# Optimization experiments

Hardware: AMD Instinct MI355X
Metric: run time of the kernel (lower is better)

The kernel has to match this reference:

```python
import jax, jax.numpy as jnp
import numpy as np

B, N, C, P = 16, 4096, 4, 64
D = 128        # conv output channels (fixed in module)
WIN = 7        # window_size
ALPHA = 0.5
EPS = 1e-5     # BatchNorm eps


def setup_inputs() -> dict:
    key = jax.random.key(0)
    k1, k2, k3, k4 = jax.random.split(key, 4)
    x = jax.random.normal(k1, (B, N, C, P), jnp.float32)
    x_template = jax.random.normal(k2, (B, N, C, P), jnp.float32)
    # Conv1d(n_channel, 128, kernel_size=n_pts): weight [128, C, P], bias [128]
    W = jax.random.normal(k3, (D, C, P), jnp.float32) * 0.05
    b = jax.random.normal(k4, (D,), jnp.float32) * 0.01
    gamma = jnp.ones((D,), jnp.float32)   # BN weight init = 1
    beta = jnp.zeros((D,), jnp.float32)   # BN bias init = 0
    return {"x": x, "x_template": x_template, "W": W, "b": b, "gamma": gamma, "beta": beta}


def _embed(x_flat, W, b, gamma, beta):
    # Conv1d with kernel_size == full length -> contraction over (C, P), output length 1.
    h = jnp.einsum('ncp,dcp->nd', x_flat, W) + b           # [B*N, D]
    # BatchNorm1d in training mode: per-channel stats over the (B*N, L=1) batch.
    mean = h.mean(axis=0)
    var = h.var(axis=0)                                     # biased variance (torch BN)
    h = (h - mean) / jnp.sqrt(var + EPS) * gamma + beta
    return jnp.where(h >= 0, h, 0.1 * h)                    # LeakyReLU(0.1)


def reference(x, x_template, W, b, gamma, beta):
    nb, nc, ch, npt = x.shape
    hw = WIN // 2
    off = jnp.arange(-hw, hw + 1)
    raw = jnp.arange(nc)[:, None] + off[None, :]
    valid = (raw >= 0) & (raw < nc)                         # dedups clamped edge cols (matches dense mask)
    cols = jnp.clip(raw, 0, nc - 1)

    emb_x = _embed(x.reshape(nb * nc, ch, npt), W, b, gamma, beta).reshape(nb, nc, D)
    emb_t = _embed(x_template.reshape(nb * nc, ch, npt), W, b, gamma, beta).reshape(nb, nc, D)

    # Banded similarity: only the window entries the module actually uses.
    emb_t_win = emb_t[:, cols]
    sim = jnp.einsum('bnd,bnwd->bnw', emb_x, emb_t_win)

    # feat_fused = raw sim gathered at clamped window inds (duplicates at edges kept)
    feat_fused = sim

    # Masked softmax over the window (invalid = clamped duplicates excluded, as in dense mask)
    mx = jnp.where(valid, sim, -jnp.inf).max(axis=-1, keepdims=True)
    e = jnp.where(valid, jnp.exp(sim - mx), 0.0)
    attn = e / e.sum(axis=-1, keepdims=True)

    xt_flat = x_template.reshape(nb, nc, ch * npt)
    out = jnp.einsum('bnw,bnwe->bne', attn, xt_flat[:, cols])  # [B, N, C*P]
    out = out.reshape(nb, nc, ch, npt)
    out = ALPHA * x + (1.0 - ALPHA) * out
    return out, feat_fused
```

## Files before the change

### kernel.cpp

```cpp
#include <hip/hip_runtime.h>
#include <math.h>

#define BB 16
#define NN 4096
#define DD 128
#define KK 256
#define NROWS (BB*NN)
#define WIN 7
#define HWIN 3
#define ALPHA 0.5f
#define EPS 1e-5f

typedef __attribute__((ext_vector_type(8))) short bf16x8;
typedef __attribute__((ext_vector_type(4))) float f32x4;

__device__ __forceinline__ unsigned short f2b(float f) {
    unsigned u = __float_as_uint(f);
    u += 0x7FFFu + ((u >> 16) & 1u);
    return (unsigned short)(u >> 16);
}
__device__ __forceinline__ float b2f(unsigned short s) {
    return __uint_as_float(((unsigned)s) << 16);
}
__device__ __forceinline__ float b2f_lo(unsigned v) { return __uint_as_float(v << 16); }
__device__ __forceinline__ float b2f_hi(unsigned v) { return __uint_as_float(v & 0xFFFF0000u); }
__device__ __forceinline__ float lrelu(float v) { return v >= 0.f ? v : 0.1f * v; }

__global__ __launch_bounds__(256) void k_embed_mfma(
    const float* __restrict__ x,
    const float* __restrict__ xt,
    const float* __restrict__ W,
    const float* __restrict__ bvec,
    unsigned short* __restrict__ h_out,
    float* __restrict__ sums)
{
    __shared__ unsigned short Wsh[128 * 128];
    __shared__ unsigned short Xsh[64 * 128];

    const int blk  = blockIdx.x;
    const int src  = blk >> 10;
    const int tile = blk & 1023;
    const int row0 = tile * 64;
    const float* __restrict__ X = src ? xt : x;
    unsigned short* __restrict__ H = h_out + (size_t)src * NROWS * DD;

    const int t    = threadIdx.x;
    const int lane = t & 63;
    const int w    = t >> 6;
    const int wm   = w >> 1;
    const int wn   = w & 1;

    f32x4 acc[2][4];
    #pragma unroll
    for (int m = 0; m < 2; ++m)
        #pragma unroll
        for (int n = 0; n < 4; ++n)
            #pragma unroll
            for (int j = 0; j < 4; ++j) acc[m][n][j] = 0.f;

    #pragma unroll
    for (int ph = 0; ph < 2; ++ph) {
        #pragma unroll
        for (int p = 0; p < 8; ++p) {
            const int j  = t + p * 256;
            const int r  = j >> 4, k8 = j & 15;
            const float* gp = &W[(size_t)r * KK + ph * 128 + k8 * 8];
            const float4 a = *(const float4*)(gp);
            const float4 bq = *(const float4*)(gp + 4);
            uint4 v;
            v.x = (unsigned)f2b(a.x)  | ((unsigned)f2b(a.y)  << 16);
            v.y = (unsigned)f2b(a.z)  | ((unsigned)f2b(a.w)  << 16);
            v.z = (unsigned)f2b(bq.x) | ((unsigned)f2b(bq.y) << 16);
            v.w = (unsigned)f2b(bq.z) | ((unsigned)f2b(bq.w) << 16);
            const int off = r * 256 + ((k8 * 16) ^ ((r & 7) << 4));
            *(uint4*)((char*)Wsh + off) = v;
        }
        #pragma unroll
        for (int p = 0; p < 4; ++p) {
            const int j  = t + p * 256;
            const int r  = j >> 4, k8 = j & 15;
            const float* gp = &X[(size_t)(row0 + r) * KK + ph * 128 + k8 * 8];
            const float4 a = *(const float4*)(gp);
            const float4 bq = *(const float4*)(gp + 4);
            uint4 v;
            v.x = (unsigned)f2b(a.x)  | ((unsigned)f2b(a.y)  << 16);
            v.y = (unsigned)f2b(a.z)  | ((unsigned)f2b(a.w)  << 16);
            v.z = (unsigned)f2b(bq.x) | ((unsigned)f2b(bq.y) << 16);
            v.w = (unsigned)f2b(bq.z) | ((unsigned)f2b(bq.w) << 16);
            const int off = r * 256 + ((k8 * 16) ^ ((r & 7) << 4));
            *(uint4*)((char*)Xsh + off) = v;
        }
        __syncthreads();

        #pragma unroll
        for (int kk = 0; kk < 4; ++kk) {
            const int kb = kk * 64 + ((lane >> 4) << 4);
            bf16x8 af[2], bfr[4];
            #pragma unroll
            for (int m = 0; m < 2; ++m) {
                const int r = 32 * wm + 16 * m + (lane & 15);
                af[m] = *(const bf16x8*)((const char*)Xsh + r * 256 + (kb ^ ((r & 7) << 4)));
            }
            #pragma unroll
            for (int n = 0; n < 4; ++n) {
                const int d = 64 * wn + 16 * n + (lane & 15);
                bfr[n] = *(const bf16x8*)((const char*)Wsh + d * 256 + (kb ^ ((d & 7) << 4)));
            }
            #pragma unroll
            for (int m = 0; m < 2; ++m)
                #pragma unroll
                for (int n = 0; n < 4; ++n)
                    acc[m][n] = __builtin_amdgcn_mfma_f32_16x16x32_bf16(af[m], bfr[n], acc[m][n], 0, 0, 0);
        }
        __syncthreads();
    }

    const int csub = (lane & 15);
    float bv[4];
    #pragma unroll
    for (int n = 0; n < 4; ++n) bv[n] = bvec[64 * wn + 16 * n + csub];

    float s[4] = {0.f, 0.f, 0.f, 0.f}, q[4] = {0.f, 0.f, 0.f, 0.f};
    #pragma unroll
    for (int m = 0; m < 2; ++m) {
        #pragma unroll
        for (int j = 0; j < 4; ++j) {
            const int row = row0 + 32 * wm + 16 * m + ((lane >> 4) << 2) + j;
            #pragma unroll
            for (int n = 0; n < 4; ++n) {
                const float v = acc[m][n][j] + bv[n];
                H[(size_t)row * DD + 64 * wn + 16 * n + csub] = f2b(v);
                s[n] += v;
                q[n] += v * v;
            }
        }
    }
    #pragma unroll
    for (int n = 0; n < 4; ++n) {
        s[n] += __shfl_xor(s[n], 16); s[n] += __shfl_xor(s[n], 32);
        q[n] += __shfl_xor(q[n], 16); q[n] += __shfl_xor(q[n], 32);
    }
    float* red = (float*)Xsh;
    if (lane < 16) {
        #pragma unroll
        for (int n = 0; n < 4; ++n) {
            red[w * 64 + n * 16 + lane]       = s[n];
            red[256 + w * 64 + n * 16 + lane] = q[n];
        }
    }
    __syncthreads();
    if (t < 128) {
        const int c = t, i = c & 63, vn = c >> 6;
        const float S = red[vn * 64 + i] + red[(2 + vn) * 64 + i];
        const float Q = red[256 + vn * 64 + i] + red[256 + (2 + vn) * 64 + i];
        atomicAdd(&sums[src * 256 + c], S);
        atomicAdd(&sums[src * 256 + 128 + c], Q);
    }
}

__global__ void k_stats(const float* __restrict__ sums,
                        const float* __restrict__ gamma,
                        const float* __restrict__ beta,
                        float* __restrict__ ss)
{
    const int t = threadIdx.x;
    if (t < 256) {
        const int src = t >> 7;
        const int d   = t & 127;
        const float invn = 1.0f / (float)NROWS;
        const float mean = sums[src * 256 + d] * invn;
        const float var  = sums[src * 256 + 128 + d] * invn - mean * mean;
        const float sc   = gamma[d] / sqrtf(var + EPS);
        const float sh   = beta[d] - mean * sc;
        ss[src * 256 + d]       = sc;
        ss[src * 256 + 128 + d] = sh;
    }
}

__global__ __launch_bounds__(256) void k_attn(
    const float* __restrict__ x,
    const float* __restrict__ xt,
    const unsigned short* __restrict__ h,
    const float* __restrict__ ss,
    float* __restrict__ out,
    float* __restrict__ feat)
{
    const int blk  = blockIdx.x;
    const int bb   = blk >> 7;
    const int tile = blk & 127;
    const int n0   = tile * 32;
    const int t    = threadIdx.x;

    __shared__ float ex[32][132];
    __shared__ float et[38][132];
    __shared__ float attn[32][8];

    const unsigned short* __restrict__ Hx = h;
    const unsigned short* __restrict__ Ht = h + (size_t)NROWS * DD;
    const size_t rowbase = (size_t)bb * NN;

    #pragma unroll
    for (int p = 0; p < 2; ++p) {
        const int j = t + p * 256;
        const int r = j >> 4, c8 = j & 15;
        const uint4 u = *(const uint4*)(&Hx[(rowbase + n0 + r) * DD + c8 * 8]);
        const float4 sca = *(const float4*)(&ss[c8 * 8]);
        const float4 scb = *(const float4*)(&ss[c8 * 8 + 4]);
        const float4 sha = *(const float4*)(&ss[128 + c8 * 8]);
        const float4 shb = *(const float4*)(&ss[128 + c8 * 8 + 4]);
        float* dst = &ex[r][c8 * 8];
        dst[0] = lrelu(b2f_lo(u.x) * sca.x + sha.x);
        dst[1] = lrelu(b2f_hi(u.x) * sca.y + sha.y);
        dst[2] = lrelu(b2f_lo(u.y) * sca.z + sha.z);
        dst[3] = lrelu(b2f_hi(u.y) * sca.w + sha.w);
        dst[4] = lrelu(b2f_lo(u.z) * scb.x + shb.x);
        dst[5] = lrelu(b2f_hi(u.z) * scb.y + shb.y);
        dst[6] = lrelu(b2f_lo(u.w) * scb.z + shb.z);
        dst[7] = lrelu(b2f_hi(u.w) * scb.w + shb.w);
    }
    #pragma unroll
    for (int p = 0; p < 3; ++p) {
        const int j = t + p * 256;
        if (j < 608) {
            const int r = j >> 4, c8 = j & 15;
            int g = n0 - HWIN + r;
            g = min(max(g, 0), NN - 1);
            const uint4 u = *(const uint4*)(&Ht[(rowbase + g) * DD + c8 * 8]);
            const float4 sca = *(const float4*)(&ss[256 + c8 * 8]);
            const float4 scb = *(const float4*)(&ss[256 + c8 * 8 + 4]);
            const float4 sha = *(const float4*)(&ss[384 + c8 * 8]);
            const float4 shb = *(const float4*)(&ss[384 + c8 * 8 + 4]);
            float* dst = &et[r][c8 * 8];
            dst[0] = lrelu(b2f_lo(u.x) * sca.x + sha.x);
            dst[1] = lrelu(b2f_hi(u.x) * sca.y + sha.y);
            dst[2] = lrelu(b2f_lo(u.y) * sca.z + sha.z);
            dst[3] = lrelu(b2f_hi(u.y) * sca.w + sha.w);
            dst[4] = lrelu(b2f_lo(u.z) * scb.x + shb.x);
            dst[5] = lrelu(b2f_hi(u.z) * scb.y + shb.y);
            dst[6] = lrelu(b2f_lo(u.w) * scb.z + shb.z);
            dst[7] = lrelu(b2f_hi(u.w) * scb.w + shb.w);
        }
    }
    __syncthreads();

    if (t < 224) {
        const int n_i = t / 7;
        const int wv  = t % 7;
        const float* a = &ex[n_i][0];
        const float* b = &et[n_i + wv][0];
        float acc = 0.f;
        #pragma unroll
        for (int d4 = 0; d4 < 128; d4 += 4) {
            const float4 av = *(const float4*)(a + d4);
            const float4 bv = *(const float4*)(b + d4);
            acc += av.x * bv.x + av.y * bv.y + av.z * bv.z + av.w * bv.w;
        }
        feat[(rowbase + n0 + n_i) * WIN + wv] = acc;
        attn[n_i][wv] = acc;
    }
    __syncthreads();

    if (t < 32) {
        const int n = n0 + t;
        float mx = -1e30f;
        #pragma unroll
        for (int wv = 0; wv < WIN; ++wv) {
            const int c = n + wv - HWIN;
            if (c >= 0 && c < NN) mx = fmaxf(mx, attn[t][wv]);
        }
        float e[WIN];
        float esum = 0.f;
        #pragma unroll
        for (int wv = 0; wv < WIN; ++wv) {
            const int c = n + wv - HWIN;
            const bool valid = (c >= 0 && c < NN);
            e[wv] = valid ? expf(attn[t][wv] - mx) : 0.f;
            esum += e[wv];
        }
        const float inv = 1.0f / esum;
        #pragma unroll
        for (int wv = 0; wv < WIN; ++wv) attn[t][wv] = e[wv] * inv;
    }
    __syncthreads();

    #pragma unroll
    for (int p = 0; p < 8; ++p) {
        const int idx = t + p * 256;
        const int n_i = idx >> 6, e4 = idx & 63;
        const int n = n0 + n_i;
        const float4 xv = *(const float4*)(&x[(rowbase + n) * KK + e4 * 4]);
        float4 acc = make_float4(0.f, 0.f, 0.f, 0.f);
        #pragma unroll
        for (int wv = 0; wv < WIN; ++wv) {
            int g = n + wv - HWIN;
            g = min(max(g, 0), NN - 1);
            const float aw = attn[n_i][wv];
            const float4 tv = *(const float4*)(&xt[(rowbase + g) * KK + e4 * 4]);
            acc.x += aw * tv.x;
            acc.y += aw * tv.y;
            acc.z += aw * tv.z;
            acc.w += aw * tv.w;
        }
        float4 o;
        o.x = ALPHA * xv.x + (1.f - ALPHA) * acc.x;
        o.y = ALPHA * xv.y + (1.f - ALPHA) * acc.y;
        o.z = ALPHA * xv.z + (1.f - ALPHA) * acc.z;
        o.w = ALPHA * xv.w + (1.f - ALPHA) * acc.w;
        *(float4*)(&out[(rowbase + n) * KK + e4 * 4]) = o;
    }
}

extern "C" void kernel_launch(void* const* d_in, const int* in_sizes, int n_in,
                              void* d_out, int out_size, void* d_ws, size_t ws_size,
                              hipStream_t stream) {
    const float* x     = (const float*)d_in[0];
    const float* xt    = (const float*)d_in[1];
    const float* W     = (const float*)d_in[2];
    const float* bvec  = (const float*)d_in[3];
    const float* gamma = (const float*)d_in[4];
    const float* beta  = (const float*)d_in[5];

    float* out  = (float*)d_out;
    float* feat = out + (size_t)BB * NN * KK;

    char*  ws   = (char*)d_ws;
    unsigned short* h = (unsigned short*)ws;
    float* sums = (float*)(ws + (size_t)33554432);
    float* ss   = (float*)(ws + (size_t)33556480);

    hipMemsetAsync(sums, 0, 512 * sizeof(float), stream);
    k_embed_mfma<<<2048, 256, 0, stream>>>(x, xt, W, bvec, h, sums);
    k_stats<<<1, 256, 0, stream>>>(sums, gamma, beta, ss);
    k_attn<<<2048, 256, 0, stream>>>(x, xt, h, ss, out, feat);
}
```

Before: 237.5 us.

## Persistent double-buffered embed GEMM with register-resident weights; stage template in LDS

A small prep kernel converts W to swizzled bf16 once. The embed kernel now runs 256 blocks of 512 threads. Each block keeps its W fragments in registers and loops over eight 64-row X tiles, staging the next tile into a second LDS buffer while it computes the current one. This removes the per-block repeated W conversion and cuts the atomic count. In the attention kernel, the template rows for the window are staged once into LDS as bf16, overlapped with the softmax warp. This replaces seven redundant global fp32 reads per output element, but it lowers the precision of the weighted sum to bf16.

```diff
diff --git a/kernel.cpp b/kernel.cpp
--- a/kernel.cpp
+++ b/kernel.cpp
@@ -19,142 +19,161 @@
     u += 0x7FFFu + ((u >> 16) & 1u);
     return (unsigned short)(u >> 16);
 }
-__device__ __forceinline__ float b2f(unsigned short s) {
-    return __uint_as_float(((unsigned)s) << 16);
-}
 __device__ __forceinline__ float b2f_lo(unsigned v) { return __uint_as_float(v << 16); }
 __device__ __forceinline__ float b2f_hi(unsigned v) { return __uint_as_float(v & 0xFFFF0000u); }
 __device__ __forceinline__ float lrelu(float v) { return v >= 0.f ? v : 0.1f * v; }
 
-__global__ __launch_bounds__(256) void k_embed_mfma(
+__device__ __forceinline__ uint4 pack8(float4 a, float4 b) {
+    uint4 v;
+    v.x = (unsigned)f2b(a.x)  | ((unsigned)f2b(a.y)  << 16);
+    v.y = (unsigned)f2b(a.z)  | ((unsigned)f2b(a.w)  << 16);
+    v.z = (unsigned)f2b(b.x)  | ((unsigned)f2b(b.y)  << 16);
+    v.w = (unsigned)f2b(b.z)  | ((unsigned)f2b(b.w)  << 16);
+    return v;
+}
+
+__global__ __launch_bounds__(256) void k_prep(
+    const float* __restrict__ W, unsigned char* __restrict__ Wswz)
+{
+    const int id = blockIdx.x * 256 + threadIdx.x;
+    const int d  = id >> 5, c8 = id & 31;
+    const float4 a = *(const float4*)(&W[(size_t)d * KK + c8 * 8]);
+    const float4 b = *(const float4*)(&W[(size_t)d * KK + c8 * 8 + 4]);
+    const int off = d * 512 + ((c8 * 16) ^ ((d & 7) << 4));
+    *(uint4*)(Wswz + off) = pack8(a, b);
+}
+
+__device__ __forceinline__ void stage_x(const float* __restrict__ X, int grow0,
+                                        unsigned short* dst, int t)
+{
+    #pragma unroll
+    for (int p = 0; p < 4; ++p) {
+        const int j  = t + p * 512;
+        const int r  = j >> 5, c8 = j & 31;
+        const float* gp = X + (size_t)(grow0 + r) * KK + c8 * 8;
+        const float4 a = *(const float4*)(gp);
+        const float4 b = *(const float4*)(gp + 4);
+        const int off = r * 512 + ((c8 * 16) ^ ((r & 7) << 4));
+        *(uint4*)((char*)dst + off) = pack8(a, b);
+    }
+}
+
+__global__ __launch_bounds__(512) void k_embed(
     const float* __restrict__ x,
     const float* __restrict__ xt,
-    const float* __restrict__ W,
+    const uint4* __restrict__ Wswz,
     const float* __restrict__ bvec,
     unsigned short* __restrict__ h_out,
     float* __restrict__ sums)
 {
-    __shared__ unsigned short Wsh[128 * 128];
-    __shared__ unsigned short Xsh[64 * 128];
+    __shared__ unsigned short Wsh[128 * 256];
+    __shared__ unsigned short Xs[2][64 * 256];
 
     const int blk  = blockIdx.x;
-    const int src  = blk >> 10;
-    const int tile = blk & 1023;
-    const int row0 = tile * 64;
+    const int src  = blk >> 7;
+    const int tile = blk & 127;
+    const int row0 = tile * 512;
     const float* __restrict__ X = src ? xt : x;
     unsigned short* __restrict__ H = h_out + (size_t)src * NROWS * DD;
 
     const int t    = threadIdx.x;
     const int lane = t & 63;
     const int w    = t >> 6;
-    const int wm   = w >> 1;
-    const int wn   = w & 1;
-
-    f32x4 acc[2][4];
-    #pragma unroll
-    for (int m = 0; m < 2; ++m)
-        #pragma unroll
-        for (int n = 0; n < 4; ++n)
+    const int wm   = w & 1;
+    const int wn   = w >> 1;
+    const int l15  = lane & 15;
+    const int lg   = lane >> 4;
+
+    {
+        uint4* d4 = (uint4*)Wsh;
+        #pragma unroll
+        for (int p = 0; p < 8; ++p) d4[t + p * 512] = Wswz[t + p * 512];
+    }
+    stage_x(X, row0, &Xs[0][0], t);
+    __syncthreads();
+
+    bf16x8 breg[2][8];
+    #pragma unroll
+    for (int n = 0; n < 2; ++n) {
+        const int d = 32 * wn + 16 * n + l15;
+        #pragma unroll
+        for (int k = 0; k < 8; ++k) {
+            const int addr = d * 512 + (((k * 64) + lg * 16) ^ ((d & 7) << 4));
+            breg[n][k] = *(const bf16x8*)((const char*)Wsh + addr);
+        }
+    }
+
+    const float bv0 = bvec[32 * wn + l15];
+    const float bv1 = bvec[32 * wn + 16 + l15];
+    float s0 = 0.f, s1 = 0.f, q0 = 0.f, q1 = 0.f;
+
+    for (int st = 0; st < 8; ++st) {
+        const int cur = st & 1;
+        f32x4 acc[2][2];
+        #pragma unroll
+        for (int m = 0; m < 2; ++m)
             #pragma unroll
-            for (int j = 0; j < 4; ++j) acc[m][n][j] = 0.f;
-
-    #pragma unroll
-    for (int ph = 0; ph < 2; ++ph) {
-        #pragma unroll
-        for (int p = 0; p < 8; ++p) {
-            const int j  = t + p * 256;
-            const int r  = j >> 4, k8 = j & 15;
-            const float* gp = &W[(size_t)r * KK + ph * 128 + k8 * 8];
-            const float4 a = *(const float4*)(gp);
-            const float4 bq = *(const float4*)(gp + 4);
-            uint4 v;
-            v.x = (unsigned)f2b(a.x)  | ((unsigned)f2b(a.y)  << 16);
-            v.y = (unsigned)f2b(a.z)  | ((unsigned)f2b(a.w)  << 16);
-            v.z = (unsigned)f2b(bq.x) | ((unsigned)f2b(bq.y) << 16);
-            v.w = (unsigned)f2b(bq.z) | ((unsigned)f2b(bq.w) << 16);
-            const int off = r * 256 + ((k8 * 16) ^ ((r & 7) << 4));
-            *(uint4*)((char*)Wsh + off) = v;
-        }
-        #pragma unroll
-        for (int p = 0; p < 4; ++p) {
-            const int j  = t + p * 256;
-            const int r  = j >> 4, k8 = j & 15;
-            const float* gp = &X[(size_t)(row0 + r) * KK + ph * 128 + k8 * 8];
-            const float4 a = *(const float4*)(gp);
-            const float4 bq = *(const float4*)(gp + 4);
-            uint4 v;
-            v.x = (unsigned)f2b(a.x)  | ((unsigned)f2b(a.y)  << 16);
-            v.y = (unsigned)f2b(a.z)  | ((unsigned)f2b(a.w)  << 16);
-            v.z = (unsigned)f2b(bq.x) | ((unsigned)f2b(bq.y) << 16);
-            v.w = (unsigned)f2b(bq.z) | ((unsigned)f2b(bq.w) << 16);
-            const int off = r * 256 + ((k8 * 16) ^ ((r & 7) << 4));
-            *(uint4*)((char*)Xsh + off) = v;
-        }
-        __syncthreads();
-
-        #pragma unroll
-        for (int kk = 0; kk < 4; ++kk) {
-            const int kb = kk * 64 + ((lane >> 4) << 4);
-            bf16x8 af[2], bfr[4];
+            for (int n = 0; n < 2; ++n)
+                #pragma unroll
+                for (int j = 0; j < 4; ++j) acc[m][n][j] = 0.f;
+
+        const char* xb = (const char*)&Xs[cur][0];
+        #pragma unroll
+        for (int k = 0; k < 8; ++k) {
+            bf16x8 af[2];
             #pragma unroll
             for (int m = 0; m < 2; ++m) {
-                const int r = 32 * wm + 16 * m + (lane & 15);
-                af[m] = *(const bf16x8*)((const char*)Xsh + r * 256 + (kb ^ ((r & 7) << 4)));
+                const int r = 32 * wm + 16 * m + l15;
+                const int addr = r * 512 + (((k * 64) + lg * 16) ^ ((r & 7) << 4));
+                af[m] = *(const bf16x8*)(xb + addr);
             }
+            acc[0][0] = __builtin_amdgcn_mfma_f32_16x16x32_bf16(af[0], breg[0][k], acc[0][0], 0, 0, 0);
+            acc[0][1] = __builtin_amdgcn_mfma_f32_16x16x32_bf16(af[0], breg[1][k], acc[0][1], 0, 0, 0);
+            acc[1][0] = __builtin_amdgcn_mfma_f32_16x16x32_bf16(af[1], breg[0][k], acc[1][0], 0, 0, 0);
+            acc[1][1] = __builtin_amdgcn_mfma_f32_16x16x32_bf16(af[1], breg[1][k], acc[1][1], 0, 0, 0);
+        }
+
+        if (st < 7) stage_x(X, row0 + (st + 1) * 64, &Xs[cur ^ 1][0], t);
+
+        #pragma unroll
+        for (int m = 0; m < 2; ++m) {
             #pragma unroll
-            for (int n = 0; n < 4; ++n) {
-                const int d = 64 * wn + 16 * n + (lane & 15);
-                bfr[n] = *(const bf16x8*)((const char*)Wsh + d * 256 + (kb ^ ((d & 7) << 4)));
+            for (int j = 0; j < 4; ++j) {
+                const int row = row0 + st * 64 + 32 * wm + 16 * m + lg * 4 + j;
+                const float v0 = acc[m][0][j] + bv0;
+                const float v1 = acc[m][1][j] + bv1;
+                H[(size_t)row * DD + 32 * wn + l15]      = f2b(v0);
+                H[(size_t)row * DD + 32 * wn + 16 + l15] = f2b(v1);
+                s0 += v0; q0 += v0 * v0;
+                s1 += v1; q1 += v1 * v1;
             }
-            #pragma unroll
-            for (int m = 0; m < 2; ++m)
-                #pragma unroll
-                for (int n = 0; n < 4; ++n)
-                    acc[m][n] = __builtin_amdgcn_mfma_f32_16x16x32_bf16(af[m], bfr[n], acc[m][n], 0, 0, 0);
         }
         __syncthreads();
     }
 
-    const int csub = (lane & 15);
-    float bv[4];
-    #pragma unroll
-    for (int n = 0; n < 4; ++n) bv[n] = bvec[64 * wn + 16 * n + csub];
-
-    float s[4] = {0.f, 0.f, 0.f, 0.f}, q[4] = {0.f, 0.f, 0.f, 0.f};
-    #pragma unroll
-    for (int m = 0; m < 2; ++m) {
-        #pragma unroll
-        for (int j = 0; j < 4; ++j) {
-            const int row = row0 + 32 * wm + 16 * m + ((lane >> 4) << 2) + j;
-            #pragma unroll
-            for (int n = 0; n < 4; ++n) {
-                const float v = acc[m][n][j] + bv[n];
-                H[(size_t)row * DD + 64 * wn + 16 * n + csub] = f2b(v);
-                s[n] += v;
-                q[n] += v * v;
-            }
-        }
-    }
-    #pragma unroll
-    for (int n = 0; n < 4; ++n) {
-        s[n] += __shfl_xor(s[n], 16); s[n] += __shfl_xor(s[n], 32);
-        q[n] += __shfl_xor(q[n], 16); q[n] += __shfl_xor(q[n], 32);
-    }
-    float* red = (float*)Xsh;
+    s0 += __shfl_xor(s0, 16); s0 += __shfl_xor(s0, 32);
+    s1 += __shfl_xor(s1, 16); s1 += __shfl_xor(s1, 32);
+    q0 += __shfl_xor(q0, 16); q0 += __shfl_xor(q0, 32);
+    q1 += __shfl_xor(q1, 16); q1 += __shfl_xor(q1, 32);
+    float* red = (float*)Wsh;
     if (lane < 16) {
-        #pragma unroll
-        for (int n = 0; n < 4; ++n) {
-            red[w * 64 + n * 16 + lane]       = s[n];
-            red[256 + w * 64 + n * 16 + lane] = q[n];
-        }
+        red[(w * 2 + 0) * 16 + l15]       = s0;
+        red[(w * 2 + 1) * 16 + l15]       = s1;
+        red[256 + (w * 2 + 0) * 16 + l15] = q0;
+        red[256 + (w * 2 + 1) * 16 + l15] = q1;
     }
     __syncthreads();
     if (t < 128) {
-        const int c = t, i = c & 63, vn = c >> 6;
-        const float S = red[vn * 64 + i] + red[(2 + vn) * 64 + i];
-        const float Q = red[256 + vn * 64 + i] + red[256 + (2 + vn) * 64 + i];
-        atomicAdd(&sums[src * 256 + c], S);
-        atomicAdd(&sums[src * 256 + 128 + c], Q);
+        const int wn_ = t >> 5, n_ = (t >> 4) & 1, li = t & 15;
+        float S = 0.f, Q = 0.f;
+        #pragma unroll
+        for (int wm_ = 0; wm_ < 2; ++wm_) {
+            const int w_ = wn_ * 2 + wm_;
+            S += red[(w_ * 2 + n_) * 16 + li];
+            Q += red[256 + (w_ * 2 + n_) * 16 + li];
+        }
+        atomicAdd(&sums[src * 256 + t], S);
+        atomicAdd(&sums[src * 256 + 128 + t], Q);
     }
 }
 
@@ -193,7 +212,7 @@
 
     __shared__ float ex[32][132];
     __shared__ float et[38][132];
-    __shared__ float attn[32][8];
+    __shared__ float attnw[32][8];
 
     const unsigned short* __restrict__ Hx = h;
     const unsigned short* __restrict__ Ht = h + (size_t)NROWS * DD;
@@ -256,17 +275,33 @@
             acc += av.x * bv.x + av.y * bv.y + av.z * bv.z + av.w * bv.w;
         }
         feat[(rowbase + n0 + n_i) * WIN + wv] = acc;
-        attn[n_i][wv] = acc;
-    }
-    __syncthreads();
-
-    if (t < 32) {
-        const int n = n0 + t;
+        attnw[n_i][wv] = acc;
+    }
+    __syncthreads();
+
+    unsigned short* xts = (unsigned short*)&et[0][0];
+    if (t < 224) {
+        #pragma unroll
+        for (int p = 0; p < 6; ++p) {
+            const int j = t + p * 224;
+            if (j < 1216) {
+                const int r = j >> 5, c8 = j & 31;
+                int g = n0 - HWIN + r;
+                g = min(max(g, 0), NN - 1);
+                const float* gp = &xt[(rowbase + g) * KK + c8 * 8];
+                const float4 a = *(const float4*)(gp);
+                const float4 b = *(const float4*)(gp + 4);
+                *(uint4*)((char*)xts + r * 512 + c8 * 16) = pack8(a, b);
+            }
+        }
+    } else {
+        const int n_i = t - 224;
+        const int n = n0 + n_i;
         float mx = -1e30f;
         #pragma unroll
         for (int wv = 0; wv < WIN; ++wv) {
             const int c = n + wv - HWIN;
-            if (c >= 0 && c < NN) mx = fmaxf(mx, attn[t][wv]);
+            if (c >= 0 && c < NN) mx = fmaxf(mx, attnw[n_i][wv]);
         }
         float e[WIN];
         float esum = 0.f;
@@ -274,12 +309,12 @@
         for (int wv = 0; wv < WIN; ++wv) {
             const int c = n + wv - HWIN;
             const bool valid = (c >= 0 && c < NN);
-            e[wv] = valid ? expf(attn[t][wv] - mx) : 0.f;
+            e[wv] = valid ? expf(attnw[n_i][wv] - mx) : 0.f;
             esum += e[wv];
         }
         const float inv = 1.0f / esum;
         #pragma unroll
-        for (int wv = 0; wv < WIN; ++wv) attn[t][wv] = e[wv] * inv;
+        for (int wv = 0; wv < WIN; ++wv) attnw[n_i][wv] = e[wv] * inv;
     }
     __syncthreads();
 
@@ -292,14 +327,12 @@
         float4 acc = make_float4(0.f, 0.f, 0.f, 0.f);
         #pragma unroll
         for (int wv = 0; wv < WIN; ++wv) {
-            int g = n + wv - HWIN;
-            g = min(max(g, 0), NN - 1);
-            const float aw = attn[n_i][wv];
-            const float4 tv = *(const float4*)(&xt[(rowbase + g) * KK + e4 * 4]);
-            acc.x += aw * tv.x;
-            acc.y += aw * tv.y;
-            acc.z += aw * tv.z;
-            acc.w += aw * tv.w;
+            const float aw = attnw[n_i][wv];
+            const uint2 u = *(const uint2*)((const char*)xts + (n_i + wv) * 512 + e4 * 8);
+            acc.x += aw * b2f_lo(u.x);
+            acc.y += aw * b2f_hi(u.x);
+            acc.z += aw * b2f_lo(u.y);
+            acc.w += aw * b2f_hi(u.y);
         }
         float4 o;
         o.x = ALPHA * xv.x + (1.f - ALPHA) * acc.x;
@@ -323,13 +356,15 @@
     float* out  = (float*)d_out;
     float* feat = out + (size_t)BB * NN * KK;
 
-    char*  ws   = (char*)d_ws;
-    unsigned short* h = (unsigned short*)ws;
-    float* sums = (float*)(ws + (size_t)33554432);
-    float* ss   = (float*)(ws + (size_t)33556480);
+    char* ws = (char*)d_ws;
+    unsigned short* h  = (unsigned short*)ws;
+    float* sums        = (float*)(ws + 33554432);
+    float* ss          = (float*)(ws + 33556480);
+    unsigned char* Wsz = (unsigned char*)(ws + 33558528);
 
     hipMemsetAsync(sums, 0, 512 * sizeof(float), stream);
-    k_embed_mfma<<<2048, 256, 0, stream>>>(x, xt, W, bvec, h, sums);
+    k_prep<<<16, 256, 0, stream>>>(W, Wsz);
+    k_embed<<<256, 512, 0, stream>>>(x, xt, (const uint4*)Wsz, bvec, h, sums);
     k_stats<<<1, 256, 0, stream>>>(sums, gamma, beta, ss);
     k_attn<<<2048, 256, 0, stream>>>(x, xt, h, ss, out, feat);
 }
```

Result: faster. 221.0 us (-6.9%).
